# Kernel tuning notes

Hardware: AMD Instinct MI355X
Metric: run time of the kernel (lower is better)

The kernel has to match this reference:

```python
import jax, jax.numpy as jnp
import numpy as np

B, S, E = 2, 2048, 2048
H, KV, D = 32, 8, 128
EPS = 1e-6


def _rope_tables(seq_len, head_dim, base=1_000_000.0):
    inv_freq = 1.0 / (base ** (np.arange(0, head_dim, 2, dtype=np.float32) / head_dim))
    ang = np.arange(seq_len, dtype=np.float32)[:, None] * inv_freq[None, :]  # [S, D/2]
    cos = np.concatenate([np.cos(ang), np.cos(ang)], axis=-1)  # [S, D]
    sin = np.concatenate([np.sin(ang), np.sin(ang)], axis=-1)
    return jnp.asarray(cos), jnp.asarray(sin)


def setup_inputs() -> dict:
    key = jax.random.key(0)
    ks = jax.random.split(key, 8)
    x = jax.random.normal(ks[0], (B, S, E), dtype=jnp.float32)
    mask = jnp.triu(jnp.ones((S, S), dtype=bool), k=1)  # True = masked (causal)
    cos, sin = _rope_tables(S, D)
    w = 0.02
    Wq = jax.random.normal(ks[1], (E, H * D), dtype=jnp.float32) * w
    bq = jnp.zeros((H * D,), dtype=jnp.float32)
    Wk = jax.random.normal(ks[2], (E, KV * D), dtype=jnp.float32) * w
    bk = jnp.zeros((KV * D,), dtype=jnp.float32)
    Wv = jax.random.normal(ks[3], (E, KV * D), dtype=jnp.float32) * w
    bv = jnp.zeros((KV * D,), dtype=jnp.float32)
    Wo = jax.random.normal(ks[4], (H * D, E), dtype=jnp.float32) * w
    q_scale = jnp.ones((D,), dtype=jnp.float32)
    k_scale = jnp.ones((D,), dtype=jnp.float32)
    return {"x": x, "mask": mask, "cos": cos, "sin": sin, "Wq": Wq, "bq": bq,
            "Wk": Wk, "bk": bk, "Wv": Wv, "bv": bv, "Wo": Wo,
            "q_scale": q_scale, "k_scale": k_scale}


def _rmsnorm(x, scale):
    xf = x.astype(jnp.float32)
    var = jnp.mean(xf * xf, axis=-1, keepdims=True)
    return (xf * jax.lax.rsqrt(var + EPS) * scale).astype(x.dtype)


def _apply_rope(x, cos, sin):
    # x: [B, h, S, D]; cos/sin: [S, D]
    d2 = x.shape[-1] // 2
    x1, x2 = x[..., :d2], x[..., d2:]
    rotated = jnp.concatenate([-x2, x1], axis=-1)
    return (x * cos[None, None] + rotated * sin[None, None]).astype(x.dtype)


def reference(x, mask, cos, sin, Wq, bq, Wk, bk, Wv, bv, Wo, q_scale, k_scale):
    b, s, _ = x.shape
    q = (x @ Wq + bq).reshape(b, s, H, D).transpose(0, 2, 1, 3)   # [B,H,S,D]
    k = (x @ Wk + bk).reshape(b, s, KV, D).transpose(0, 2, 1, 3)  # [B,KV,S,D]
    v = (x @ Wv + bv).reshape(b, s, KV, D).transpose(0, 2, 1, 3)
    q = _rmsnorm(q, q_scale)
    k = _rmsnorm(k, k_scale)
    q = _apply_rope(q, cos, sin)
    k = _apply_rope(k, cos, sin)
    group = H // KV
    k = jnp.repeat(k, group, axis=1)  # repeat_interleave on head dim -> [B,H,S,D]
    v = jnp.repeat(v, group, axis=1)
    scores = jnp.einsum("bhqd,bhkd->bhqk", q, k)
    scores = jnp.where(mask[None, None], -jnp.inf, scores)
    attn = jax.nn.softmax(scores / jnp.sqrt(jnp.float32(D)), axis=-1)
    ctx = jnp.einsum("bhqk,bhkd->bhqd", attn, v)
    ctx = ctx.transpose(0, 2, 1, 3).reshape(b, s, H * D)
    return ctx @ Wo
```

## Files before the change

kernel.cpp:

```cpp
#include <hip/hip_runtime.h>

typedef short short8 __attribute__((ext_vector_type(8)));
typedef float f32x4 __attribute__((ext_vector_type(4)));
typedef float f32x16 __attribute__((ext_vector_type(16)));
typedef unsigned int uint2v __attribute__((ext_vector_type(2)));

static __device__ __forceinline__ ushort f2bf(float f){
  union { float f; uint u; } cv; cv.f = f;
  uint u = cv.u;
  uint r = (u + 0x7fffu + ((u >> 16) & 1u)) >> 16;
  return (ushort)r;
}
static __device__ __forceinline__ float bf2f(ushort h){
  union { uint u; float f; } cv; cv.u = ((uint)h) << 16; return cv.f;
}
static __device__ __forceinline__ f32x4 mfma16x16x32(short8 a, short8 b, f32x4 c){
  return __builtin_amdgcn_mfma_f32_16x16x32_bf16(a, b, c, 0, 0, 0);
}
static __device__ __forceinline__ f32x16 mfma32(short8 a, short8 b, f32x16 c){
  return __builtin_amdgcn_mfma_f32_32x32x16_bf16(a, b, c, 0, 0, 0);
}
static __device__ __forceinline__ float ex2(float x){
  float r; asm("v_exp_f32 %0, %1" : "=v"(r) : "v"(x)); return r;
}
static __device__ __forceinline__ uint cvtpk(float lo, float hi){
  uint r; asm("v_cvt_pk_bf16_f32 %0, %1, %2" : "=v"(r) : "v"(lo), "v"(hi)); return r;
}
static __device__ __forceinline__ void glds16(const void* g, const void* l){
  __builtin_amdgcn_global_load_lds((const __attribute__((address_space(1))) void*)g,
                                   (__attribute__((address_space(3))) void*)l, 16, 0, 0);
}
static __device__ __forceinline__ void store_out(float* p, float v){ *p = v; }
static __device__ __forceinline__ void store_out(ushort* p, float v){ *p = f2bf(v); }
static __device__ __forceinline__ int xcd_swizzle(int flat, int nwg){
  int q = nwg >> 3, r = nwg & 7;
  int xcd = flat & 7, idx = flat >> 3;
  return (xcd < r) ? xcd * (q + 1) + idx : r * (q + 1) + (xcd - r) * q + idx;
}

__global__ void cvt_bf16_kernel(const float* __restrict__ x, ushort* __restrict__ y, int n4){
  int i = blockIdx.x * 256 + threadIdx.x;
  if (i < n4){
    float4 v = reinterpret_cast<const float4*>(x)[i];
    ushort4 o; o.x = f2bf(v.x); o.y = f2bf(v.y); o.z = f2bf(v.z); o.w = f2bf(v.w);
    reinterpret_cast<ushort4*>(y)[i] = o;
  }
}

__global__ void addk_kernel(const float* __restrict__ p0, const float* __restrict__ p1,
                            float* __restrict__ out, int n4){
  int i = blockIdx.x * 256 + threadIdx.x;
  if (i < n4){
    float4 a = reinterpret_cast<const float4*>(p0)[i];
    float4 b = reinterpret_cast<const float4*>(p1)[i];
    float4 o; o.x = a.x + b.x; o.y = a.y + b.y; o.z = a.z + b.z; o.w = a.w + b.w;
    reinterpret_cast<float4*>(out)[i] = o;
  }
}

__global__ void transpose_cvt_kernel(const float* __restrict__ W, ushort* __restrict__ WT, int K, int N){
  __shared__ float tile[32][33];
  int n0 = blockIdx.x * 32, k0 = blockIdx.y * 32;
  int tx = threadIdx.x, ty = threadIdx.y;
  #pragma unroll
  for (int i = 0; i < 4; i++){ int r = ty + i * 8; tile[r][tx] = W[(size_t)(k0 + r) * N + n0 + tx]; }
  __syncthreads();
  #pragma unroll
  for (int i = 0; i < 4; i++){ int r = ty + i * 8; WT[(size_t)(n0 + r) * K + k0 + tx] = f2bf(tile[tx][r]); }
}

__global__ void bias_concat_kernel(const float* __restrict__ bq, const float* __restrict__ bk,
                                   const float* __restrict__ bv, float* __restrict__ out){
  int i = blockIdx.x * 256 + threadIdx.x;
  if (i < 6144) out[i] = (i < 4096) ? bq[i] : ((i < 5120) ? bk[i - 4096] : bv[i - 5120]);
}

template<typename OutT>
__global__ __launch_bounds__(512, 2) void gemm256_kernel(const ushort* __restrict__ A, const ushort* __restrict__ BT,
                                                         const float* __restrict__ bias, OutT* __restrict__ C,
                                                         int M, int N, int K, int klen){
  __shared__ __align__(16) ushort As[2][256 * 64];
  __shared__ __align__(16) ushort Bs[2][256 * 64];
  const int nbx = N >> 8;
  const int nwg = nbx * (M >> 8);
  const int wg = xcd_swizzle(blockIdx.x, nwg);
  const int m0 = (wg / nbx) * 256, n0 = (wg % nbx) * 256;
  const int kb = blockIdx.y * klen;
  OutT* Cp = C + (size_t)blockIdx.y * M * N;
  const int tid = threadIdx.x, w = tid >> 6, l = tid & 63, lm = l & 15, lk = l >> 4;
  const int wr = w >> 2, wc = w & 3;
  const int sr = tid >> 3, sc = tid & 7;
  const int scs = sc ^ (sr & 7);
  const int swz = lm & 7;
  const int nt = klen >> 6;
  const size_t abase = (size_t)(m0 + sr) * K + kb + scs * 8;
  const size_t bbase = (size_t)(n0 + sr) * K + kb + scs * 8;

#define STG_P(T, BUF, P) do{                                                                    \
    glds16(A  + abase + (size_t)(2*(P))  *64*K + (T)*64, &As[BUF][(2*(P))  *4096 + w*512]);     \
    glds16(A  + abase + (size_t)(2*(P)+1)*64*K + (T)*64, &As[BUF][(2*(P)+1)*4096 + w*512]);     \
    glds16(BT + bbase + (size_t)(2*(P))  *64*K + (T)*64, &Bs[BUF][(2*(P))  *4096 + w*512]);     \
    glds16(BT + bbase + (size_t)(2*(P)+1)*64*K + (T)*64, &Bs[BUF][(2*(P)+1)*4096 + w*512]);     \
  }while(0)

#define RD_A(DST, RD, MB) do{                                                                   \
    _Pragma("unroll")                                                                           \
    for (int mi = 0; mi < 4; mi++)                                                              \
      _Pragma("unroll")                                                                         \
      for (int ks = 0; ks < 2; ks++)                                                            \
        DST[mi][ks] = *(const short8*)&As[RD][(wr*128 + ((MB)+mi)*16 + lm)*64 + (((ks*4+lk)^swz)*8)]; \
  }while(0)
#define RD_B(DST, RD, NB) do{                                                                   \
    _Pragma("unroll")                                                                           \
    for (int ni = 0; ni < 2; ni++)                                                              \
      _Pragma("unroll")                                                                         \
      for (int ks = 0; ks < 2; ks++)                                                            \
        DST[ni][ks] = *(const short8*)&Bs[RD][(wc*64 + ((NB)+ni)*16 + lm)*64 + (((ks*4+lk)^swz)*8)]; \
  }while(0)
#define MM(MB, NB, AF, BF) do{                                                                  \
    __builtin_amdgcn_s_setprio(1);                                                             \
    _Pragma("unroll")                                                                           \
    for (int mi = 0; mi < 4; mi++)                                                              \
      _Pragma("unroll")                                                                         \
      for (int ni = 0; ni < 2; ni++)                                                            \
        _Pragma("unroll")                                                                       \
        for (int ks = 0; ks < 2; ks++)                                                          \
          acc[(MB)+mi][(NB)+ni] = mfma16x16x32(AF[mi][ks], BF[ni][ks], acc[(MB)+mi][(NB)+ni]); \
    __builtin_amdgcn_s_setprio(0);                                                             \
  }while(0)

  f32x4 acc[8][4] = {};
  STG_P(0, 0, 0); STG_P(0, 0, 1);
  for (int t = 0; t < nt; t++){
    const int rd = t & 1, wb = rd ^ 1;
    const bool pf = (t + 1 < nt);
    if (pf) STG_P(t + 1, wb, 0);
    if (pf) asm volatile("s_waitcnt vmcnt(4)" ::: "memory");
    else    asm volatile("s_waitcnt vmcnt(0)" ::: "memory");
    __builtin_amdgcn_s_barrier();
    short8 af[4][2], bf01[2][2], bf23[2][2];
    RD_A(af, rd, 0); RD_B(bf01, rd, 0);
    __builtin_amdgcn_s_barrier();
    MM(0, 0, af, bf01);
    __builtin_amdgcn_s_barrier();
    RD_B(bf23, rd, 2);
    if (pf) STG_P(t + 1, wb, 1);
    __builtin_amdgcn_s_barrier();
    MM(0, 2, af, bf23);
    __builtin_amdgcn_s_barrier();
    RD_A(af, rd, 4);
    __builtin_amdgcn_s_barrier();
    MM(4, 2, af, bf23);
    __builtin_amdgcn_s_barrier();
    MM(4, 0, af, bf01);
  }
#undef STG_P
#undef RD_A
#undef RD_B
#undef MM
  #pragma unroll
  for (int mi = 0; mi < 8; mi++)
    #pragma unroll
    for (int ni = 0; ni < 4; ni++){
      int col = n0 + wc * 64 + ni * 16 + lm;
      float bb = bias ? bias[col] : 0.0f;
      #pragma unroll
      for (int r = 0; r < 4; r++){
        int row = m0 + wr * 128 + mi * 16 + lk * 4 + r;
        store_out(&Cp[(size_t)row * N + col], acc[mi][ni][r] + bb);
      }
    }
}

#define QSCL2 0.12752016f
__global__ __launch_bounds__(256) void norm_rope_kernel(const ushort* __restrict__ qkv,
    const float* __restrict__ cosT, const float* __restrict__ sinT,
    const float* __restrict__ qs, const float* __restrict__ ksc,
    ushort* __restrict__ qo, ushort* __restrict__ ko, ushort* __restrict__ vto){
  int slot = blockIdx.x * 4 + (threadIdx.x >> 6);
  int lane = threadIdx.x & 63;
  int row = slot / 48, c = slot % 48;
  int b = row >> 11, s = row & 2047;
  size_t base = (size_t)row * 6144 + c * 128;
  float e1 = bf2f(qkv[base + lane]);
  float e2 = bf2f(qkv[base + lane + 64]);
  if (c < 40){
    float ss = e1 * e1 + e2 * e2;
    #pragma unroll
    for (int m = 1; m < 64; m <<= 1) ss += __shfl_xor(ss, m);
    float rs = rsqrtf(ss * (1.0f / 128.0f) + 1e-6f);
    const float* sc = (c < 32) ? qs : ksc;
    float n1 = e1 * rs * sc[lane], n2 = e2 * rs * sc[lane + 64];
    float c1 = cosT[s * 128 + lane],      s1 = sinT[s * 128 + lane];
    float c2 = cosT[s * 128 + lane + 64], s2 = sinT[s * 128 + lane + 64];
    float o1 = n1 * c1 - n2 * s1;
    float o2 = n2 * c2 + n1 * s2;
    if (c < 32){
      size_t ob = ((size_t)(b * 32 + c) * 2048 + s) * 128;
      qo[ob + lane] = f2bf(o1 * QSCL2); qo[ob + lane + 64] = f2bf(o2 * QSCL2);
    } else {
      int kv = c - 32;
      size_t ob = ((size_t)(b * 8 + kv) * 2048 + s) * 128;
      ko[ob + lane] = f2bf(o1); ko[ob + lane + 64] = f2bf(o2);
    }
  } else {
    int kv = c - 40;
    size_t ob = (size_t)(b * 8 + kv) * 128;
    vto[(ob + lane) * 2048 + s]      = f2bf(e1);
    vto[(ob + lane + 64) * 2048 + s] = f2bf(e2);
  }
}

__global__ __launch_bounds__(256, 2) void flash_kernel(const ushort* __restrict__ Q, const ushort* __restrict__ Kg,
    const ushort* __restrict__ VTg, ushort* __restrict__ ctx){
  __shared__ ushort Kl[2][64 * 128];
  __shared__ ushort Vl[2][128 * 64];
  const int bh = blockIdx.y, b = bh >> 5, h = bh & 31, kvh = h >> 2;
  const int bx = blockIdx.x;
  const int tid = threadIdx.x, w = tid >> 6, l = tid & 63;
  const int q31 = l & 31, hi = l >> 5, swz = q31 & 7;
  const ushort* Kbase = Kg  + (size_t)(b * 8 + kvh) * 2048 * 128;
  const ushort* Vbase = VTg + (size_t)(b * 8 + kvh) * 128 * 2048;
  const int krow = l >> 4, kcol = l & 15;
  const int vrow = l >> 3, vcol = l & 7;

  #define STAGE(KT, BS) do {                                                            \
    _Pragma("unroll")                                                                   \
    for (int i2 = 0; i2 < 4; i2++){                                                     \
      int i = w * 4 + i2; int row = i * 4 + krow;                                       \
      glds16(Kbase + (size_t)((KT) * 64 + row) * 128 + ((kcol ^ (row & 7)) * 8),        \
             &Kl[BS][i * 512]);                                                         \
    }                                                                                   \
    _Pragma("unroll")                                                                   \
    for (int j2 = 0; j2 < 4; j2++){                                                     \
      int j = w * 4 + j2; int row = j * 8 + vrow;                                       \
      glds16(Vbase + (size_t)row * 2048 + (KT) * 64 + ((vcol ^ (row & 7)) * 8),         \
             &Vl[BS][j * 512]);                                                         \
    }                                                                                   \
  } while (0)

  for (int pass = 0; pass < 2; pass++){
    const int qb = pass ? bx : (15 - bx);
    const int q0 = qb * 128;
    const int qw = q0 + w * 32;
    const int myq = qw + q31;
    const ushort* Qp = Q + ((size_t)(b * 32 + h) * 2048 + myq) * 128;
    short8 qf[8];
    #pragma unroll
    for (int s = 0; s < 8; s++) qf[s] = *(const short8*)(Qp + s * 16 + hi * 8);
    f32x16 o[4] = {};
    float m_r = -INFINITY, l_r = 0.f;
    const int nt = 2 * qb + 2;

    STAGE(0, 0);
    for (int kt = 0; kt < nt; kt++){
      const int cur = kt & 1;
      if (kt + 1 < nt){
        STAGE(kt + 1, cur ^ 1);
        asm volatile("s_waitcnt vmcnt(8)" ::: "memory");
      } else {
        asm volatile("s_waitcnt vmcnt(0)" ::: "memory");
      }
      __builtin_amdgcn_s_barrier();
      asm volatile("" ::: "memory");
      f32x16 sa0 = {}, sa1 = {};
      __builtin_amdgcn_s_setprio(1);
      #pragma unroll
      for (int s = 0; s < 8; s++){
        short8 a0 = *(const short8*)&Kl[cur][q31 * 128 + (((2 * s + hi) ^ swz) * 8)];
        short8 a1 = *(const short8*)&Kl[cur][(32 + q31) * 128 + (((2 * s + hi) ^ swz) * 8)];
        sa0 = mfma32(a0, qf[s], sa0);
        sa1 = mfma32(a1, qf[s], sa1);
      }
      __builtin_amdgcn_s_setprio(0);
      if (kt >= 2 * qb){
        #pragma unroll
        for (int r = 0; r < 16; r++){
          int krel = (r & 3) + 8 * (r >> 2) + 4 * hi;
          if (kt * 64 + krel > myq)      sa0[r] = -INFINITY;
          if (kt * 64 + 32 + krel > myq) sa1[r] = -INFINITY;
        }
      }
      float mx = fmaxf(sa0[0], sa1[0]);
      #pragma unroll
      for (int r = 1; r < 16; r++) mx = fmaxf(mx, fmaxf(sa0[r], sa1[r]));
      mx = fmaxf(mx, __shfl_xor(mx, 32));
      if (!__all(mx - m_r <= 8.f)){
        float mn = fmaxf(m_r, mx);
        float al = ex2(m_r - mn);
        m_r = mn; l_r *= al;
        #pragma unroll
        for (int r = 0; r < 16; r++){
          float alq = __shfl(al, (r & 3) + 8 * (r >> 2) + 4 * hi);
          o[0][r] *= alq; o[1][r] *= alq; o[2][r] *= alq; o[3][r] *= alq;
        }
      }
      float rsum = 0.f;
      #pragma unroll
      for (int r = 0; r < 16; r++){
        sa0[r] = ex2(sa0[r] - m_r);
        sa1[r] = ex2(sa1[r] - m_r);
        rsum += sa0[r] + sa1[r];
      }
      rsum += __shfl_xor(rsum, 32);
      l_r += rsum;
      uint pk0[8], pk1[8];
      #pragma unroll
      for (int t = 0; t < 8; t++){
        pk0[t] = cvtpk(sa0[2 * t], sa0[2 * t + 1]);
        pk1[t] = cvtpk(sa1[2 * t], sa1[2 * t + 1]);
      }
      __builtin_amdgcn_s_setprio(1);
      #pragma unroll
      for (int sub = 0; sub < 2; sub++){
        #pragma unroll
        for (int kc = 0; kc < 2; kc++){
          uint p0 = sub ? pk1[4 * kc]     : pk0[4 * kc];
          uint p1 = sub ? pk1[4 * kc + 1] : pk0[4 * kc + 1];
          uint p2 = sub ? pk1[4 * kc + 2] : pk0[4 * kc + 2];
          uint p3 = sub ? pk1[4 * kc + 3] : pk0[4 * kc + 3];
          uint2v r02 = __builtin_amdgcn_permlane32_swap(p0, p2, false, false);
          uint2v r13 = __builtin_amdgcn_permlane32_swap(p1, p3, false, false);
          union { uint u[4]; short8 v; } Af;
          Af.u[0] = r02[0]; Af.u[1] = r13[0]; Af.u[2] = r02[1]; Af.u[3] = r13[1];
          #pragma unroll
          for (int dc = 0; dc < 4; dc++){
            short8 vf = *(const short8*)&Vl[cur][(dc * 32 + q31) * 64 + (((4 * sub + 2 * kc + hi) ^ swz) * 8)];
            o[dc] = mfma32(Af.v, vf, o[dc]);
          }
        }
      }
      __builtin_amdgcn_s_setprio(0);
      asm volatile("" ::: "memory");
      __builtin_amdgcn_s_barrier();
    }
    float invl = 1.0f / l_r;
    ushort* Cp = ctx + (size_t)(b * 2048 + qw) * 4096 + (size_t)h * 128;
    #pragma unroll
    for (int r = 0; r < 16; r++){
      int qrel = (r & 3) + 8 * (r >> 2) + 4 * hi;
      float inv = __shfl(invl, qrel);
      #pragma unroll
      for (int dc = 0; dc < 4; dc++)
        Cp[(size_t)qrel * 4096 + dc * 32 + q31] = f2bf(o[dc][r] * inv);
    }
  }
  #undef STAGE
}

extern "C" void kernel_launch(void* const* d_in, const int* in_sizes, int n_in,
                              void* d_out, int out_size, void* d_ws, size_t ws_size,
                              hipStream_t stream){
  const float* x    = (const float*)d_in[0];
  const float* cosT = (const float*)d_in[2];
  const float* sinT = (const float*)d_in[3];
  const float* Wq   = (const float*)d_in[4];
  const float* bq   = (const float*)d_in[5];
  const float* Wk   = (const float*)d_in[6];
  const float* bk   = (const float*)d_in[7];
  const float* Wv   = (const float*)d_in[8];
  const float* bv   = (const float*)d_in[9];
  const float* Wo   = (const float*)d_in[10];
  const float* qs   = (const float*)d_in[11];
  const float* ksc  = (const float*)d_in[12];
  float* out = (float*)d_out;
  char* ws = (char*)d_ws;

  ushort* xb    = (ushort*)(ws + 0);
  ushort* wtqkv = (ushort*)(ws + 16777216);
  float*  biasq = (float* )(ws + 41943040);
  ushort* qkv   = (ushort*)(ws + 41967616);
  ushort* qb_   = (ushort*)(ws + 92299264);
  ushort* kb_   = (ushort*)(ws + 125853696);
  ushort* vtb   = (ushort*)(ws + 134242304);
  ushort* ctx   = (ushort*)(ws + 142630912);
  ushort* wot   = (ushort*)(ws + 176185344);
  float* part   = (float*)(ws + 41967616);

  cvt_bf16_kernel<<<8192, 256, 0, stream>>>(x, xb, 2097152);
  transpose_cvt_kernel<<<dim3(128, 64), dim3(32, 8), 0, stream>>>(Wq, wtqkv, 2048, 4096);
  transpose_cvt_kernel<<<dim3(32, 64),  dim3(32, 8), 0, stream>>>(Wk, wtqkv + (size_t)4096 * 2048, 2048, 1024);
  transpose_cvt_kernel<<<dim3(32, 64),  dim3(32, 8), 0, stream>>>(Wv, wtqkv + (size_t)5120 * 2048, 2048, 1024);
  transpose_cvt_kernel<<<dim3(64, 128), dim3(32, 8), 0, stream>>>(Wo, wot, 4096, 2048);
  bias_concat_kernel<<<24, 256, 0, stream>>>(bq, bk, bv, biasq);

  gemm256_kernel<ushort><<<dim3(384, 1), 512, 0, stream>>>(xb, wtqkv, biasq, qkv, 4096, 6144, 2048, 2048);
  norm_rope_kernel<<<49152, 256, 0, stream>>>(qkv, cosT, sinT, qs, ksc, qb_, kb_, vtb);
  flash_kernel<<<dim3(8, 64), 256, 0, stream>>>(qb_, kb_, vtb, ctx);
  gemm256_kernel<float><<<dim3(128, 2), 512, 0, stream>>>(ctx, wot, nullptr, part, 4096, 2048, 4096, 2048);
  addk_kernel<<<8192, 256, 0, stream>>>(part, part + (size_t)4096 * 2048, out, 2097152);
}
```

Before: 418.5 us.

## Rewrite GEMM to 32x32x16 MFMA with quarter-tile staged 8-phase pipeline

Both projection GEMMs now issue 32x32x16 bf16 MFMAs on 32-row fragments instead of 16x16x32, with fewer, larger LDS reads per fragment. Global-to-LDS staging is split into four quarter loads (A/B halves) spread across the eight phases of each k-step, with barriers in between. The aim is more work per MFMA issue and less LDS read traffic per flop. Launch bounds drop from 2 to 1 block per CU and more barriers are added, which may reduce latency hiding.

```diff
diff --git a/kernel.cpp b/kernel.cpp
--- a/kernel.cpp
+++ b/kernel.cpp
@@ -13,9 +13,6 @@
 }
 static __device__ __forceinline__ float bf2f(ushort h){
   union { uint u; float f; } cv; cv.u = ((uint)h) << 16; return cv.f;
-}
-static __device__ __forceinline__ f32x4 mfma16x16x32(short8 a, short8 b, f32x4 c){
-  return __builtin_amdgcn_mfma_f32_16x16x32_bf16(a, b, c, 0, 0, 0);
 }
 static __device__ __forceinline__ f32x16 mfma32(short8 a, short8 b, f32x16 c){
   return __builtin_amdgcn_mfma_f32_32x32x16_bf16(a, b, c, 0, 0, 0);
@@ -76,98 +73,102 @@
 }
 
 template<typename OutT>
-__global__ __launch_bounds__(512, 2) void gemm256_kernel(const ushort* __restrict__ A, const ushort* __restrict__ BT,
-                                                         const float* __restrict__ bias, OutT* __restrict__ C,
-                                                         int M, int N, int K, int klen){
-  __shared__ __align__(16) ushort As[2][256 * 64];
-  __shared__ __align__(16) ushort Bs[2][256 * 64];
+__global__ __launch_bounds__(512, 1) void gemm8p_kernel(const ushort* __restrict__ A, const ushort* __restrict__ BT,
+                                                        const float* __restrict__ bias, OutT* __restrict__ C,
+                                                        int M, int N, int K, int klen){
+  __shared__ __align__(16) ushort As[2][2][128 * 64];
+  __shared__ __align__(16) ushort Bs[2][2][128 * 64];
   const int nbx = N >> 8;
   const int nwg = nbx * (M >> 8);
   const int wg = xcd_swizzle(blockIdx.x, nwg);
   const int m0 = (wg / nbx) * 256, n0 = (wg % nbx) * 256;
   const int kb = blockIdx.y * klen;
   OutT* Cp = C + (size_t)blockIdx.y * M * N;
-  const int tid = threadIdx.x, w = tid >> 6, l = tid & 63, lm = l & 15, lk = l >> 4;
+  const int tid = threadIdx.x, w = tid >> 6, l = tid & 63;
+  const int l31 = l & 31, hi = l >> 5, swz = l31 & 7;
   const int wr = w >> 2, wc = w & 3;
-  const int sr = tid >> 3, sc = tid & 7;
-  const int scs = sc ^ (sr & 7);
-  const int swz = lm & 7;
+  const int bhalf = wc >> 1, brow0 = (wc & 1) * 64;
+  const int srow = tid >> 3, schunk = tid & 7;
+  const int sg = schunk ^ (srow & 7);
   const int nt = klen >> 6;
-  const size_t abase = (size_t)(m0 + sr) * K + kb + scs * 8;
-  const size_t bbase = (size_t)(n0 + sr) * K + kb + scs * 8;
-
-#define STG_P(T, BUF, P) do{                                                                    \
-    glds16(A  + abase + (size_t)(2*(P))  *64*K + (T)*64, &As[BUF][(2*(P))  *4096 + w*512]);     \
-    glds16(A  + abase + (size_t)(2*(P)+1)*64*K + (T)*64, &As[BUF][(2*(P)+1)*4096 + w*512]);     \
-    glds16(BT + bbase + (size_t)(2*(P))  *64*K + (T)*64, &Bs[BUF][(2*(P))  *4096 + w*512]);     \
-    glds16(BT + bbase + (size_t)(2*(P)+1)*64*K + (T)*64, &Bs[BUF][(2*(P)+1)*4096 + w*512]);     \
+
+#define STG(MAT, H, T, BUF) do{                                                            \
+    const ushort* _s = (MAT) ? BT : A;                                                     \
+    const int _rb = ((MAT) ? n0 : m0) + (H) * 128;                                         \
+    ushort* _d = (MAT) ? &Bs[BUF][H][0] : &As[BUF][H][0];                                  \
+    glds16(_s + (size_t)(_rb + srow) * K + kb + (size_t)(T) * 64 + sg * 8,                 \
+           _d + (w * 64) * 8);                                                             \
+    glds16(_s + (size_t)(_rb + 64 + srow) * K + kb + (size_t)(T) * 64 + sg * 8,            \
+           _d + (512 + w * 64) * 8);                                                       \
   }while(0)
 
-#define RD_A(DST, RD, MB) do{                                                                   \
-    _Pragma("unroll")                                                                           \
-    for (int mi = 0; mi < 4; mi++)                                                              \
-      _Pragma("unroll")                                                                         \
-      for (int ks = 0; ks < 2; ks++)                                                            \
-        DST[mi][ks] = *(const short8*)&As[RD][(wr*128 + ((MB)+mi)*16 + lm)*64 + (((ks*4+lk)^swz)*8)]; \
+#define RD_AF(BUF, MTB) do{                                                                \
+    _Pragma("unroll")                                                                      \
+    for (int mt2 = 0; mt2 < 2; mt2++)                                                      \
+      _Pragma("unroll")                                                                    \
+      for (int ks = 0; ks < 4; ks++)                                                       \
+        afr[mt2][ks] = *(const short8*)&As[BUF][wr]                                        \
+            [(((MTB) + mt2) * 32 + l31) * 64 + (((ks * 2 + hi) ^ swz) * 8)];               \
   }while(0)
-#define RD_B(DST, RD, NB) do{                                                                   \
-    _Pragma("unroll")                                                                           \
-    for (int ni = 0; ni < 2; ni++)                                                              \
-      _Pragma("unroll")                                                                         \
-      for (int ks = 0; ks < 2; ks++)                                                            \
-        DST[ni][ks] = *(const short8*)&Bs[RD][(wc*64 + ((NB)+ni)*16 + lm)*64 + (((ks*4+lk)^swz)*8)]; \
+
+#define RD_BF(DST, BUF, NT) do{                                                            \
+    _Pragma("unroll")                                                                      \
+    for (int ks = 0; ks < 4; ks++)                                                         \
+      DST[ks] = *(const short8*)&Bs[BUF][bhalf]                                            \
+          [(brow0 + (NT) * 32 + l31) * 64 + (((ks * 2 + hi) ^ swz) * 8)];                  \
   }while(0)
-#define MM(MB, NB, AF, BF) do{                                                                  \
-    __builtin_amdgcn_s_setprio(1);                                                             \
-    _Pragma("unroll")                                                                           \
-    for (int mi = 0; mi < 4; mi++)                                                              \
-      _Pragma("unroll")                                                                         \
-      for (int ni = 0; ni < 2; ni++)                                                            \
-        _Pragma("unroll")                                                                       \
-        for (int ks = 0; ks < 2; ks++)                                                          \
-          acc[(MB)+mi][(NB)+ni] = mfma16x16x32(AF[mi][ks], BF[ni][ks], acc[(MB)+mi][(NB)+ni]); \
-    __builtin_amdgcn_s_setprio(0);                                                             \
+
+#define MM(MTB, NT, BF) do{                                                                \
+    __builtin_amdgcn_s_setprio(1);                                                        \
+    _Pragma("unroll")                                                                      \
+    for (int mt2 = 0; mt2 < 2; mt2++)                                                      \
+      _Pragma("unroll")                                                                    \
+      for (int ks = 0; ks < 4; ks++)                                                       \
+        acc[(MTB) + mt2][NT] = mfma32(afr[mt2][ks], BF[ks], acc[(MTB) + mt2][NT]);         \
+    __builtin_amdgcn_s_setprio(0);                                                        \
   }while(0)
 
-  f32x4 acc[8][4] = {};
-  STG_P(0, 0, 0); STG_P(0, 0, 1);
+  f32x16 acc[4][2] = {};
+  short8 afr[2][4], bfr0[4], bfr1[4];
+  STG(0, 0, 0, 0); STG(1, 0, 0, 0); STG(0, 1, 0, 0); STG(1, 1, 0, 0);
   for (int t = 0; t < nt; t++){
-    const int rd = t & 1, wb = rd ^ 1;
+    const int buf = t & 1, nb = buf ^ 1;
     const bool pf = (t + 1 < nt);
-    if (pf) STG_P(t + 1, wb, 0);
-    if (pf) asm volatile("s_waitcnt vmcnt(4)" ::: "memory");
-    else    asm volatile("s_waitcnt vmcnt(0)" ::: "memory");
-    __builtin_amdgcn_s_barrier();
-    short8 af[4][2], bf01[2][2], bf23[2][2];
-    RD_A(af, rd, 0); RD_B(bf01, rd, 0);
-    __builtin_amdgcn_s_barrier();
-    MM(0, 0, af, bf01);
-    __builtin_amdgcn_s_barrier();
-    RD_B(bf23, rd, 2);
-    if (pf) STG_P(t + 1, wb, 1);
-    __builtin_amdgcn_s_barrier();
-    MM(0, 2, af, bf23);
-    __builtin_amdgcn_s_barrier();
-    RD_A(af, rd, 4);
-    __builtin_amdgcn_s_barrier();
-    MM(4, 2, af, bf23);
-    __builtin_amdgcn_s_barrier();
-    MM(4, 0, af, bf01);
-  }
-#undef STG_P
-#undef RD_A
-#undef RD_B
+    if (pf){ STG(0, 0, t + 1, nb); asm volatile("s_waitcnt vmcnt(2)" ::: "memory"); }
+    else   { asm volatile("s_waitcnt vmcnt(0)" ::: "memory"); }
+    __builtin_amdgcn_s_barrier();
+    RD_AF(buf, 0); RD_BF(bfr0, buf, 0);
+    MM(0, 0, bfr0);
+    __builtin_amdgcn_s_barrier();
+    RD_BF(bfr1, buf, 1);
+    if (pf) STG(1, 0, t + 1, nb);
+    __builtin_amdgcn_s_barrier();
+    MM(0, 1, bfr1);
+    __builtin_amdgcn_s_barrier();
+    RD_AF(buf, 2);
+    if (pf) STG(0, 1, t + 1, nb);
+    __builtin_amdgcn_s_barrier();
+    MM(2, 1, bfr1);
+    __builtin_amdgcn_s_barrier();
+    if (pf) STG(1, 1, t + 1, nb);
+    __builtin_amdgcn_s_barrier();
+    MM(2, 0, bfr0);
+    __builtin_amdgcn_s_barrier();
+  }
+#undef STG
+#undef RD_AF
+#undef RD_BF
 #undef MM
   #pragma unroll
-  for (int mi = 0; mi < 8; mi++)
+  for (int mt = 0; mt < 4; mt++)
     #pragma unroll
-    for (int ni = 0; ni < 4; ni++){
-      int col = n0 + wc * 64 + ni * 16 + lm;
+    for (int ntl = 0; ntl < 2; ntl++){
+      int col = n0 + wc * 64 + ntl * 32 + l31;
       float bb = bias ? bias[col] : 0.0f;
       #pragma unroll
-      for (int r = 0; r < 4; r++){
-        int row = m0 + wr * 128 + mi * 16 + lk * 4 + r;
-        store_out(&Cp[(size_t)row * N + col], acc[mi][ni][r] + bb);
+      for (int reg = 0; reg < 16; reg++){
+        int row = m0 + wr * 128 + mt * 32 + (reg & 3) + 8 * (reg >> 2) + 4 * hi;
+        store_out(&Cp[(size_t)row * N + col], acc[mt][ntl][reg] + bb);
       }
     }
 }
@@ -384,9 +385,9 @@
   transpose_cvt_kernel<<<dim3(64, 128), dim3(32, 8), 0, stream>>>(Wo, wot, 4096, 2048);
   bias_concat_kernel<<<24, 256, 0, stream>>>(bq, bk, bv, biasq);
 
-  gemm256_kernel<ushort><<<dim3(384, 1), 512, 0, stream>>>(xb, wtqkv, biasq, qkv, 4096, 6144, 2048, 2048);
+  gemm8p_kernel<ushort><<<dim3(384, 1), 512, 0, stream>>>(xb, wtqkv, biasq, qkv, 4096, 6144, 2048, 2048);
   norm_rope_kernel<<<49152, 256, 0, stream>>>(qkv, cosT, sinT, qs, ksc, qb_, kb_, vtb);
   flash_kernel<<<dim3(8, 64), 256, 0, stream>>>(qb_, kb_, vtb, ctx);
-  gemm256_kernel<float><<<dim3(128, 2), 512, 0, stream>>>(ctx, wot, nullptr, part, 4096, 2048, 4096, 2048);
+  gemm8p_kernel<float><<<dim3(128, 2), 512, 0, stream>>>(ctx, wot, nullptr, part, 4096, 2048, 4096, 2048);
   addk_kernel<<<8192, 256, 0, stream>>>(part, part + (size_t)4096 * 2048, out, 2097152);
 }
```

Result: no change. 417.3 us (-0.3%).
